# Kernel tuning notes

Measured on AMD Instinct MI355X. Metric: run time of the kernel, lower is better.

The kernel has to match this reference:

```python
import jax, jax.numpy as jnp
import numpy as np

N_NODES = 50000
N_EDGES = 800000
IN_DIM = 128
HID = 128
NUM_GRAPHS = 64


def setup_inputs() -> dict:
    key = jax.random.key(0)
    ks = jax.random.split(key, 10)
    x = jax.random.normal(ks[0], (N_NODES, IN_DIM), dtype=jnp.float32)
    edge_index = jax.random.randint(ks[1], (2, N_EDGES), 0, N_NODES, dtype=jnp.int64)
    batch = jnp.sort(jax.random.randint(ks[2], (N_NODES,), 0, NUM_GRAPHS, dtype=jnp.int64))
    s = 1.0 / np.sqrt(IN_DIM)
    W0 = jax.random.uniform(ks[3], (IN_DIM, HID), jnp.float32, -s, s)
    b0 = jnp.zeros((HID,), jnp.float32)
    s = 1.0 / np.sqrt(HID)
    W1 = jax.random.uniform(ks[4], (HID, HID), jnp.float32, -s, s)
    b1 = jnp.zeros((HID,), jnp.float32)
    W2 = jax.random.uniform(ks[5], (HID, HID), jnp.float32, -s, s)
    b2 = jnp.zeros((HID,), jnp.float32)
    return {"x": x, "edge_index": edge_index, "batch": batch,
            "W0": W0, "b0": b0, "W1": W1, "b1": b1, "W2": W2, "b2": b2}


def reference(x, edge_index, batch, W0, b0, W1, b1, W2, b2):
    N = x.shape[0]
    # GCNConv: add self loops, symmetric degree normalization
    loop = jnp.arange(N, dtype=edge_index.dtype)
    src = jnp.concatenate([edge_index[0], loop])  # [E+N]
    dst = jnp.concatenate([edge_index[1], loop])
    deg = jax.ops.segment_sum(jnp.ones_like(dst, dtype=x.dtype), dst, num_segments=N)
    dinv = jnp.where(deg > 0, jax.lax.rsqrt(deg), 0.0)
    norm = (dinv[src] * dinv[dst])[:, None]  # [E+N, 1]

    def gcn_layer(h, W, b):
        h = h @ W  # [N, hid]
        agg = jax.ops.segment_sum(h[src] * norm, dst, num_segments=N)
        return agg + b

    h = jax.nn.relu(gcn_layer(x, W0, b0))
    h = jax.nn.relu(gcn_layer(h, W1, b1))
    h = jax.nn.relu(gcn_layer(h, W2, b2))
    # dropout is identity at inference (training=False)

    # global_mean_pool by batch index
    sums = jax.ops.segment_sum(h, batch, num_segments=NUM_GRAPHS)
    counts = jax.ops.segment_sum(jnp.ones((N,), h.dtype), batch, num_segments=NUM_GRAPHS)
    return sums / jnp.maximum(counts, 1.0)[:, None]
```

## Files before the change

kernel.cpp:

```cpp
#include <hip/hip_runtime.h>
#include <hip/hip_bf16.h>

#define NNODES 50000
#define NEDGES 800000
#define HIDDIM 128
#define NGRAPH 64
#define BUCKET 64

typedef __attribute__((ext_vector_type(8))) short short8;
typedef __attribute__((ext_vector_type(4))) float floatx4;
typedef __attribute__((ext_vector_type(4))) unsigned short ushortx4;
typedef __attribute__((ext_vector_type(4))) unsigned int uintx4;

__device__ __forceinline__ float bfbits2f(unsigned short u) {
    return __uint_as_float(((unsigned int)u) << 16);
}
__device__ __forceinline__ unsigned short f2bfbits(float v) {
    __hip_bfloat16 h = __float2bfloat16(v);
    return __builtin_bit_cast(unsigned short, h);
}
__device__ __forceinline__ float bflo(unsigned int w) { return __uint_as_float(w << 16); }
__device__ __forceinline__ float bfhi(unsigned int w) { return __uint_as_float(w & 0xffff0000u); }

__global__ void k_detect(const unsigned int* __restrict__ xw,
                         const unsigned int* __restrict__ eiw,
                         int* __restrict__ flags) {
    __shared__ int sh_hit, sh_zero;
    int t = threadIdx.x;
    if (t == 0) { sh_hit = 0; sh_zero = 0; }
    __syncthreads();
    if (t < 128) {
        unsigned int w = xw[t * 97 + 5];
        int e = (int)((w >> 7) & 0xFF);
        if (e >= 110 && e <= 140) atomicAdd(&sh_hit, 1);
        if (eiw[1001 + 2 * t] == 0) atomicAdd(&sh_zero, 1);
    }
    __syncthreads();
    if (t == 0) {
        flags[0] = (sh_hit >= 64) ? 1 : 0;
        flags[1] = (sh_zero >= 120) ? 1 : 0;
    }
}

__global__ void k_init(const unsigned int* __restrict__ xw,
                       const unsigned int* __restrict__ eiw,
                       int* __restrict__ flags, int* __restrict__ cnt) {
    __shared__ int sh_hit, sh_zero;
    int t = threadIdx.x;
    int i = blockIdx.x * 256 + t;
    if (i < 50176) cnt[i] = 0;
    if (blockIdx.x != 0) return;
    if (t == 0) { sh_hit = 0; sh_zero = 0; }
    __syncthreads();
    if (t < 128) {
        unsigned int w = xw[t * 97 + 5];
        int e = (int)((w >> 7) & 0xFF);
        if (e >= 110 && e <= 140) atomicAdd(&sh_hit, 1);
        if (eiw[1001 + 2 * t] == 0) atomicAdd(&sh_zero, 1);
    }
    __syncthreads();
    if (t == 0) {
        flags[0] = (sh_hit >= 64) ? 1 : 0;
        flags[1] = (sh_zero >= 120) ? 1 : 0;
    }
}

__device__ __forceinline__ int ld_idx(const int* __restrict__ p, int j, int wide) {
    return wide ? p[2 * j] : p[j];
}

__global__ __launch_bounds__(256) void k_append(const int* __restrict__ ei,
                                                const int* __restrict__ bat,
                                                const int* __restrict__ flags,
                                                int* __restrict__ cnt,
                                                unsigned short* __restrict__ ecol,
                                                int* __restrict__ bounds) {
    if (blockIdx.x == gridDim.x - 1) {
        int g = threadIdx.x;
        if (g > NGRAPH) return;
        int wide = flags[1];
        int lo = 0, hi = NNODES;
        while (lo < hi) {
            int mid = (lo + hi) >> 1;
            if (ld_idx(bat, mid, wide) < g) lo = mid + 1; else hi = mid;
        }
        bounds[g] = lo;
        return;
    }
    int T = blockIdx.x * 256 + threadIdx.x;
    int e0 = T * 8;
    if (e0 >= NEDGES) return;
    int wide = flags[1];
    int s[8], d[8];
    if (wide) {
        const int4* __restrict__ sp = (const int4*)ei;
        const int4* __restrict__ dp = (const int4*)(ei + 2 * NEDGES);
#pragma unroll
        for (int q = 0; q < 4; ++q) {
            int4 sv = sp[T * 4 + q]; s[2 * q] = sv.x; s[2 * q + 1] = sv.z;
            int4 dv = dp[T * 4 + q]; d[2 * q] = dv.x; d[2 * q + 1] = dv.z;
        }
    } else {
        const int4* __restrict__ sp = (const int4*)ei;
        const int4* __restrict__ dp = (const int4*)(ei + NEDGES);
#pragma unroll
        for (int q = 0; q < 2; ++q) {
            int4 sv = sp[T * 2 + q];
            s[4 * q] = sv.x; s[4 * q + 1] = sv.y; s[4 * q + 2] = sv.z; s[4 * q + 3] = sv.w;
            int4 dv = dp[T * 2 + q];
            d[4 * q] = dv.x; d[4 * q + 1] = dv.y; d[4 * q + 2] = dv.z; d[4 * q + 3] = dv.w;
        }
    }
    int p[8];
#pragma unroll
    for (int q = 0; q < 8; ++q) p[q] = atomicAdd(&cnt[d[q]], 1);
#pragma unroll
    for (int q = 0; q < 8; ++q) {
        if (p[q] < BUCKET) {
            __builtin_nontemporal_store((unsigned short)s[q],
                                        &ecol[(size_t)d[q] * BUCKET + p[q]]);
        }
    }
}

__global__ __launch_bounds__(256) void k_gemm_mfma(const void* __restrict__ A,
                                                   const void* __restrict__ W,
                                                   const int* __restrict__ flags,
                                                   int a_mode,
                                                   const int* __restrict__ degcnt,
                                                   unsigned short* __restrict__ out,
                                                   int M) {
    __shared__ __align__(16) unsigned short Wl[16 * 128 * 8];
    __shared__ __align__(16) unsigned short Alds[64 * 17 * 8];
    const int tid = threadIdx.x;
    const int F = flags[0];
    const int abf = (a_mode == 2) ? 1 : (a_mode == 1 ? F : 0);
    const int row0 = blockIdx.x * 64;

    if (F) {
        const ushort4* __restrict__ Wg = (const ushort4*)W;
#pragma unroll
        for (int it = 0; it < 16; ++it) {
            int idx = it * 256 + tid;
            int k = idx >> 5, n = (idx & 31) * 4;
            ushort4 wv = Wg[idx];
            unsigned short* dst = &Wl[(((k >> 3) * 128) + n) * 8 + (k & 7)];
            dst[0] = wv.x; dst[8] = wv.y; dst[16] = wv.z; dst[24] = wv.w;
        }
    } else {
        const float4* __restrict__ Wg = (const float4*)W;
#pragma unroll
        for (int it = 0; it < 16; ++it) {
            int idx = it * 256 + tid;
            int k = idx >> 5, n = (idx & 31) * 4;
            float4 wv = Wg[idx];
            unsigned short* dst = &Wl[(((k >> 3) * 128) + n) * 8 + (k & 7)];
            dst[0] = f2bfbits(wv.x); dst[8]  = f2bfbits(wv.y);
            dst[16] = f2bfbits(wv.z); dst[24] = f2bfbits(wv.w);
        }
    }
    if (abf) {
#pragma unroll
        for (int it = 0; it < 4; ++it) {
            int idx = it * 256 + tid;
            int m = idx >> 4, kb = idx & 15;
            int gr = row0 + m;
            uint4 v = make_uint4(0, 0, 0, 0);
            if (gr < M) v = ((const uint4*)A)[(size_t)gr * 16 + kb];
            *reinterpret_cast<uint4*>(&Alds[(m * 17 + kb) * 8]) = v;
        }
    } else {
#pragma unroll
        for (int it = 0; it < 8; ++it) {
            int idx = it * 256 + tid;
            int m = idx >> 5, k4 = idx & 31;
            int k = k4 * 4;
            int gr = row0 + m;
            float4 v = make_float4(0, 0, 0, 0);
            if (gr < M) v = ((const float4*)A)[(size_t)gr * 32 + k4];
            ushort4 u;
            u.x = f2bfbits(v.x); u.y = f2bfbits(v.y);
            u.z = f2bfbits(v.z); u.w = f2bfbits(v.w);
            *reinterpret_cast<ushort4*>(&Alds[(m * 17 + (k >> 3)) * 8 + (k & 7)]) = u;
        }
    }
    __syncthreads();

    const int lane = tid & 63;
    const int wave = tid >> 6;
    const int q = lane >> 4;
    const int c = lane & 15;
    const int mrow = wave * 16 + c;
    floatx4 acc[8] = {};
#pragma unroll
    for (int k0 = 0; k0 < 4; ++k0) {
        int kb = k0 * 4 + q;
        short8 afrag = *reinterpret_cast<const short8*>(&Alds[(mrow * 17 + kb) * 8]);
#pragma unroll
        for (int t = 0; t < 8; ++t) {
            short8 bfrag = *reinterpret_cast<const short8*>(&Wl[(kb * 128 + t * 16 + c) * 8]);
            acc[t] = __builtin_amdgcn_mfma_f32_16x16x32_bf16(afrag, bfrag, acc[t], 0, 0, 0);
        }
    }
#pragma unroll
    for (int i = 0; i < 4; ++i) {
        int gr = row0 + wave * 16 + q * 4 + i;
        if (gr < M) {
            float s = degcnt ? rsqrtf((float)degcnt[gr] + 1.0f) : 1.0f;
#pragma unroll
            for (int t = 0; t < 8; ++t) {
                out[(size_t)gr * 128 + t * 16 + c] = f2bfbits(acc[t][i] * s);
            }
        }
    }
}

__global__ __launch_bounds__(256) void k_fused(const int* __restrict__ cnt,
                                               const unsigned short* __restrict__ ecol,
                                               const unsigned short* __restrict__ tmp16,
                                               const void* __restrict__ bias,
                                               const void* __restrict__ W,
                                               const int* __restrict__ flags,
                                               unsigned short* __restrict__ out,
                                               int M) {
    __shared__ __align__(16) unsigned short Wl[16 * 128 * 8];
    __shared__ __align__(16) unsigned short Alds[64 * 17 * 8];
    const int tid = threadIdx.x;
    const int F = flags[0];
    const int row0 = blockIdx.x * 64;

    if (F) {
        const ushort4* __restrict__ Wg = (const ushort4*)W;
#pragma unroll
        for (int it = 0; it < 16; ++it) {
            int idx = it * 256 + tid;
            int k = idx >> 5, n = (idx & 31) * 4;
            ushort4 wv = Wg[idx];
            unsigned short* dst = &Wl[(((k >> 3) * 128) + n) * 8 + (k & 7)];
            dst[0] = wv.x; dst[8] = wv.y; dst[16] = wv.z; dst[24] = wv.w;
        }
    } else {
        const float4* __restrict__ Wg = (const float4*)W;
#pragma unroll
        for (int it = 0; it < 16; ++it) {
            int idx = it * 256 + tid;
            int k = idx >> 5, n = (idx & 31) * 4;
            float4 wv = Wg[idx];
            unsigned short* dst = &Wl[(((k >> 3) * 128) + n) * 8 + (k & 7)];
            dst[0] = f2bfbits(wv.x); dst[8]  = f2bfbits(wv.y);
            dst[16] = f2bfbits(wv.z); dst[24] = f2bfbits(wv.w);
        }
    }

    {
        const uint4* __restrict__ base = reinterpret_cast<const uint4*>(tmp16);
        const int jl = tid & 15;
        const int nsub = tid >> 4;
        float b[8];
        if (F) {
            uint4 bb = ((const uint4*)bias)[jl];
            b[0] = bflo(bb.x); b[1] = bfhi(bb.x);
            b[2] = bflo(bb.y); b[3] = bfhi(bb.y);
            b[4] = bflo(bb.z); b[5] = bfhi(bb.z);
            b[6] = bflo(bb.w); b[7] = bfhi(bb.w);
        } else {
            float4 f0 = ((const float4*)bias)[2 * jl];
            float4 f1 = ((const float4*)bias)[2 * jl + 1];
            b[0] = f0.x; b[1] = f0.y; b[2] = f0.z; b[3] = f0.w;
            b[4] = f1.x; b[5] = f1.y; b[6] = f1.z; b[7] = f1.w;
        }
#pragma unroll
        for (int grp = 0; grp < 4; ++grp) {
            int m = grp * 16 + nsub;
            int n = row0 + m;
            float a[8] = {0, 0, 0, 0, 0, 0, 0, 0};
            float dn = 1.0f;
            bool live = (n < M);
            if (live) {
                int degf = cnt[n];
                dn = rsqrtf((float)degf + 1.0f);
                int deg = degf > BUCKET ? BUCKET : degf;
                const unsigned short* __restrict__ bk = &ecol[(size_t)n * BUCKET];
                uint4 u = base[(size_t)n * 16 + jl];
                a[0] = bflo(u.x); a[1] = bfhi(u.x);
                a[2] = bflo(u.y); a[3] = bfhi(u.y);
                a[4] = bflo(u.z); a[5] = bfhi(u.z);
                a[6] = bflo(u.w); a[7] = bfhi(u.w);
                int k = 0;
                for (; k + 3 < deg; k += 4) {
                    ushortx4 sv = __builtin_nontemporal_load(
                        reinterpret_cast<const ushortx4*>(&bk[k]));
                    uint4 u0 = base[(size_t)sv[0] * 16 + jl];
                    uint4 u1 = base[(size_t)sv[1] * 16 + jl];
                    uint4 u2 = base[(size_t)sv[2] * 16 + jl];
                    uint4 u3 = base[(size_t)sv[3] * 16 + jl];
                    a[0] += (bflo(u0.x) + bflo(u1.x)) + (bflo(u2.x) + bflo(u3.x));
                    a[1] += (bfhi(u0.x) + bfhi(u1.x)) + (bfhi(u2.x) + bfhi(u3.x));
                    a[2] += (bflo(u0.y) + bflo(u1.y)) + (bflo(u2.y) + bflo(u3.y));
                    a[3] += (bfhi(u0.y) + bfhi(u1.y)) + (bfhi(u2.y) + bfhi(u3.y));
                    a[4] += (bflo(u0.z) + bflo(u1.z)) + (bflo(u2.z) + bflo(u3.z));
                    a[5] += (bfhi(u0.z) + bfhi(u1.z)) + (bfhi(u2.z) + bfhi(u3.z));
                    a[6] += (bflo(u0.w) + bflo(u1.w)) + (bflo(u2.w) + bflo(u3.w));
                    a[7] += (bfhi(u0.w) + bfhi(u1.w)) + (bfhi(u2.w) + bfhi(u3.w));
                }
                for (; k < deg; ++k) {
                    uint4 u0 = base[(size_t)bk[k] * 16 + jl];
                    a[0] += bflo(u0.x); a[1] += bfhi(u0.x);
                    a[2] += bflo(u0.y); a[3] += bfhi(u0.y);
                    a[4] += bflo(u0.z); a[5] += bfhi(u0.z);
                    a[6] += bflo(u0.w); a[7] += bfhi(u0.w);
                }
            }
            unsigned int ow[4];
#pragma unroll
            for (int i2 = 0; i2 < 4; ++i2) {
                float r0 = live ? fmaxf(a[2 * i2]     * dn + b[2 * i2],     0.0f) : 0.0f;
                float r1 = live ? fmaxf(a[2 * i2 + 1] * dn + b[2 * i2 + 1], 0.0f) : 0.0f;
                ow[i2] = (unsigned int)f2bfbits(r0) | ((unsigned int)f2bfbits(r1) << 16);
            }
            *reinterpret_cast<uint4*>(&Alds[(m * 17 + jl) * 8]) =
                make_uint4(ow[0], ow[1], ow[2], ow[3]);
        }
    }
    __syncthreads();

    const int lane = tid & 63;
    const int wave = tid >> 6;
    const int q = lane >> 4;
    const int c = lane & 15;
    const int mrow = wave * 16 + c;
    floatx4 acc[8] = {};
#pragma unroll
    for (int k0 = 0; k0 < 4; ++k0) {
        int kb = k0 * 4 + q;
        short8 afrag = *reinterpret_cast<const short8*>(&Alds[(mrow * 17 + kb) * 8]);
#pragma unroll
        for (int t = 0; t < 8; ++t) {
            short8 bfrag = *reinterpret_cast<const short8*>(&Wl[(kb * 128 + t * 16 + c) * 8]);
            acc[t] = __builtin_amdgcn_mfma_f32_16x16x32_bf16(afrag, bfrag, acc[t], 0, 0, 0);
        }
    }
#pragma unroll
    for (int i = 0; i < 4; ++i) {
        int gr = row0 + wave * 16 + q * 4 + i;
        if (gr < M) {
            float s = rsqrtf((float)cnt[gr] + 1.0f);
#pragma unroll
            for (int t = 0; t < 8; ++t) {
                out[(size_t)gr * 128 + t * 16 + c] = f2bfbits(acc[t][i] * s);
            }
        }
    }
}

__global__ __launch_bounds__(256) void k_gather(const int* __restrict__ cnt,
                                                const unsigned short* __restrict__ ecol,
                                                const unsigned short* __restrict__ tmp16,
                                                const void* __restrict__ bias,
                                                const int* __restrict__ flags,
                                                unsigned short* __restrict__ outh16) {
    int t = blockIdx.x * 256 + threadIdx.x;
    int n = t >> 4;
    if (n >= NNODES) return;
    int j = t & 15;
    int degf = cnt[n];
    float dn = rsqrtf((float)degf + 1.0f);
    int deg = degf > BUCKET ? BUCKET : degf;
    const unsigned short* __restrict__ bk = &ecol[(size_t)n * BUCKET];
    const uint4* __restrict__ base = reinterpret_cast<const uint4*>(tmp16);
    float a[8];
    {
        uint4 u = base[(size_t)n * 16 + j];
        a[0] = bflo(u.x); a[1] = bfhi(u.x);
        a[2] = bflo(u.y); a[3] = bfhi(u.y);
        a[4] = bflo(u.z); a[5] = bfhi(u.z);
        a[6] = bflo(u.w); a[7] = bfhi(u.w);
    }
    int k = 0;
    for (; k + 3 < deg; k += 4) {
        ushortx4 sv = __builtin_nontemporal_load(
            reinterpret_cast<const ushortx4*>(&bk[k]));
        uint4 u0 = base[(size_t)sv[0] * 16 + j];
        uint4 u1 = base[(size_t)sv[1] * 16 + j];
        uint4 u2 = base[(size_t)sv[2] * 16 + j];
        uint4 u3 = base[(size_t)sv[3] * 16 + j];
        a[0] += (bflo(u0.x) + bflo(u1.x)) + (bflo(u2.x) + bflo(u3.x));
        a[1] += (bfhi(u0.x) + bfhi(u1.x)) + (bfhi(u2.x) + bfhi(u3.x));
        a[2] += (bflo(u0.y) + bflo(u1.y)) + (bflo(u2.y) + bflo(u3.y));
        a[3] += (bfhi(u0.y) + bfhi(u1.y)) + (bfhi(u2.y) + bfhi(u3.y));
        a[4] += (bflo(u0.z) + bflo(u1.z)) + (bflo(u2.z) + bflo(u3.z));
        a[5] += (bfhi(u0.z) + bfhi(u1.z)) + (bfhi(u2.z) + bfhi(u3.z));
        a[6] += (bflo(u0.w) + bflo(u1.w)) + (bflo(u2.w) + bflo(u3.w));
        a[7] += (bfhi(u0.w) + bfhi(u1.w)) + (bfhi(u2.w) + bfhi(u3.w));
    }
    for (; k < deg; ++k) {
        uint4 u0 = base[(size_t)bk[k] * 16 + j];
        a[0] += bflo(u0.x); a[1] += bfhi(u0.x);
        a[2] += bflo(u0.y); a[3] += bfhi(u0.y);
        a[4] += bflo(u0.z); a[5] += bfhi(u0.z);
        a[6] += bflo(u0.w); a[7] += bfhi(u0.w);
    }
    float b[8];
    if (flags[0]) {
        uint4 bb = ((const uint4*)bias)[j];
        b[0] = bflo(bb.x); b[1] = bfhi(bb.x);
        b[2] = bflo(bb.y); b[3] = bfhi(bb.y);
        b[4] = bflo(bb.z); b[5] = bfhi(bb.z);
        b[6] = bflo(bb.w); b[7] = bfhi(bb.w);
    } else {
        float4 f0 = ((const float4*)bias)[2 * j];
        float4 f1 = ((const float4*)bias)[2 * j + 1];
        b[0] = f0.x; b[1] = f0.y; b[2] = f0.z; b[3] = f0.w;
        b[4] = f1.x; b[5] = f1.y; b[6] = f1.z; b[7] = f1.w;
    }
    uintx4 ov;
#pragma unroll
    for (int i2 = 0; i2 < 4; ++i2) {
        float r0 = fmaxf(a[2 * i2]     * dn + b[2 * i2],     0.0f);
        float r1 = fmaxf(a[2 * i2 + 1] * dn + b[2 * i2 + 1], 0.0f);
        ov[i2] = (unsigned int)f2bfbits(r0) | ((unsigned int)f2bfbits(r1) << 16);
    }
    __builtin_nontemporal_store(ov,
        reinterpret_cast<uintx4*>(outh16 + (size_t)n * 128 + j * 8));
}

__global__ __launch_bounds__(256) void k_gemm(const void* __restrict__ A,
                                              const void* __restrict__ W,
                                              const int* __restrict__ flags,
                                              int a_uses_flag,
                                              float* __restrict__ out, int M) {
    __shared__ __align__(16) float Al[32 * 128];
    const int tid = threadIdx.x;
    const int F = flags[0];
    const int afmt = a_uses_flag ? F : 0;
    const int row0 = blockIdx.x * 32;
#pragma unroll
    for (int j = 0; j < 16; ++j) {
        int idx = j * 256 + tid;
        int r = idx >> 7, k = idx & 127;
        int gr = row0 + r;
        float v = 0.0f;
        if (gr < M) {
            size_t off = (size_t)gr * 128 + k;
            v = afmt ? bfbits2f(((const unsigned short*)A)[off])
                     : ((const float*)A)[off];
        }
        Al[idx] = v;
    }
    __syncthreads();
    const int tx = tid & 31, ty = tid >> 5;
    const int c0 = tx * 4;
    float acc[4][4] = {};
    if (F) {
        const ushort4* __restrict__ Wg = (const ushort4*)W;
#pragma unroll 4
        for (int k = 0; k < 128; ++k) {
            ushort4 wv = Wg[k * 32 + tx];
            float w0 = bfbits2f(wv.x), w1 = bfbits2f(wv.y);
            float w2 = bfbits2f(wv.z), w3 = bfbits2f(wv.w);
#pragma unroll
            for (int i = 0; i < 4; ++i) {
                float a = Al[(ty + i * 8) * 128 + k];
                acc[i][0] = fmaf(a, w0, acc[i][0]);
                acc[i][1] = fmaf(a, w1, acc[i][1]);
                acc[i][2] = fmaf(a, w2, acc[i][2]);
                acc[i][3] = fmaf(a, w3, acc[i][3]);
            }
        }
    } else {
        const float4* __restrict__ Wg = (const float4*)W;
#pragma unroll 4
        for (int k = 0; k < 128; ++k) {
            float4 wv = Wg[k * 32 + tx];
#pragma unroll
            for (int i = 0; i < 4; ++i) {
                float a = Al[(ty + i * 8) * 128 + k];
                acc[i][0] = fmaf(a, wv.x, acc[i][0]);
                acc[i][1] = fmaf(a, wv.y, acc[i][1]);
                acc[i][2] = fmaf(a, wv.z, acc[i][2]);
                acc[i][3] = fmaf(a, wv.w, acc[i][3]);
            }
        }
    }
#pragma unroll
    for (int i = 0; i < 4; ++i) {
        int gr = row0 + ty + i * 8;
        if (gr < M) {
            *reinterpret_cast<float4*>(&out[(size_t)gr * 128 + c0]) =
                make_float4(acc[i][0], acc[i][1], acc[i][2], acc[i][3]);
        }
    }
}
__global__ void k_deg_init(float* __restrict__ deg) {
    int i = blockIdx.x * 256 + threadIdx.x;
    if (i < NNODES) deg[i] = 1.0f;
}
__global__ void k_deg_edges(const int* __restrict__ ei, const int* __restrict__ flags,
                            float* __restrict__ deg) {
    int e = blockIdx.x * 256 + threadIdx.x;
    if (e < NEDGES) unsafeAtomicAdd(&deg[ld_idx(ei, NEDGES + e, flags[1])], 1.0f);
}
__global__ void k_rsqrt(float* __restrict__ deg) {
    int i = blockIdx.x * 256 + threadIdx.x;
    if (i < NNODES) deg[i] = 1.0f / sqrtf(deg[i]);
}
__global__ void k_selfloop(const float* __restrict__ tmp, const float* __restrict__ dinv,
                           float* __restrict__ agg) {
    int t = blockIdx.x * 256 + threadIdx.x;
    if (t >= NNODES * 32) return;
    int n = t >> 5, j = t & 31;
    float s = dinv[n]; s = s * s;
    float4 v = *reinterpret_cast<const float4*>(&tmp[(size_t)n * 128 + j * 4]);
    v.x *= s; v.y *= s; v.z *= s; v.w *= s;
    *reinterpret_cast<float4*>(&agg[(size_t)n * 128 + j * 4]) = v;
}
__global__ __launch_bounds__(256) void k_scatter(const int* __restrict__ ei,
                                                 const int* __restrict__ flags,
                                                 const float* __restrict__ dinv,
                                                 const float* __restrict__ tmp,
                                                 float* __restrict__ agg) {
    int t = blockIdx.x * 256 + threadIdx.x;
    int e = t >> 5;
    if (e >= NEDGES) return;
    int j = t & 31;
    int wide = flags[1];
    int s = ld_idx(ei, e, wide);
    int d = ld_idx(ei, NEDGES + e, wide);
    float w = dinv[s] * dinv[d];
    const float4 v = *reinterpret_cast<const float4*>(&tmp[(size_t)s * 128 + j * 4]);
    float* p = &agg[(size_t)d * 128 + j * 4];
    unsafeAtomicAdd(p + 0, v.x * w);
    unsafeAtomicAdd(p + 1, v.y * w);
    unsafeAtomicAdd(p + 2, v.z * w);
    unsafeAtomicAdd(p + 3, v.w * w);
}
__global__ void k_bias_relu(float* __restrict__ h, const void* __restrict__ b,
                            const int* __restrict__ flags) {
    int t = blockIdx.x * 256 + threadIdx.x;
    if (t >= NNODES * 32) return;
    int j = t & 31;
    float b0, b1, b2, b3;
    if (flags[0]) {
        const unsigned short* bb = (const unsigned short*)b;
        b0 = bfbits2f(bb[j * 4 + 0]); b1 = bfbits2f(bb[j * 4 + 1]);
        b2 = bfbits2f(bb[j * 4 + 2]); b3 = bfbits2f(bb[j * 4 + 3]);
    } else {
        const float* bb = (const float*)b;
        b0 = bb[j * 4 + 0]; b1 = bb[j * 4 + 1]; b2 = bb[j * 4 + 2]; b3 = bb[j * 4 + 3];
    }
    float4 v = *reinterpret_cast<float4*>(&h[(size_t)t * 4]);
    v.x = fmaxf(v.x + b0, 0.0f);
    v.y = fmaxf(v.y + b1, 0.0f);
    v.z = fmaxf(v.z + b2, 0.0f);
    v.w = fmaxf(v.w + b3, 0.0f);
    *reinterpret_cast<float4*>(&h[(size_t)t * 4]) = v;
}

__global__ void k_bounds(const int* __restrict__ batch, const int* __restrict__ flags,
                         int* __restrict__ bounds) {
    int g = threadIdx.x;
    if (g > NGRAPH) return;
    int wide = flags[1];
    int lo = 0, hi = NNODES;
    while (lo < hi) {
        int mid = (lo + hi) >> 1;
        if (ld_idx(batch, mid, wide) < g) lo = mid + 1; else hi = mid;
    }
    bounds[g] = lo;
}

__global__ __launch_bounds__(256) void k_pool_part(const unsigned short* __restrict__ h16,
                                                   const int* __restrict__ bounds,
                                                   float* __restrict__ part) {
    __shared__ float sh[256 * 4];
    int g = blockIdx.x >> 2, seg = blockIdx.x & 3;
    int t = threadIdx.x;
    int c4 = t & 31, sub = t >> 5;
    int beg = bounds[g], end = bounds[g + 1];
    const ushort4* __restrict__ base = (const ushort4*)h16;
    float ax = 0, ay = 0, az = 0, aw = 0;
    for (int r = beg + seg * 8 + sub; r < end; r += 32) {
        ushort4 u = base[(size_t)r * 32 + c4];
        ax += bfbits2f(u.x); ay += bfbits2f(u.y);
        az += bfbits2f(u.z); aw += bfbits2f(u.w);
    }
    sh[t * 4 + 0] = ax; sh[t * 4 + 1] = ay; sh[t * 4 + 2] = az; sh[t * 4 + 3] = aw;
    __syncthreads();
    if (t < 32) {
        float4 r = make_float4(0, 0, 0, 0);
#pragma unroll
        for (int s = 0; s < 8; ++s) {
            r.x += sh[(s * 32 + t) * 4 + 0];
            r.y += sh[(s * 32 + t) * 4 + 1];
            r.z += sh[(s * 32 + t) * 4 + 2];
            r.w += sh[(s * 32 + t) * 4 + 3];
        }
        *reinterpret_cast<float4*>(&part[((size_t)(g * 4 + seg)) * 128 + t * 4]) = r;
    }
}

__global__ void k_pool_final(const float* __restrict__ part, const int* __restrict__ bounds,
                             const int* __restrict__ flags, void* __restrict__ out) {
    int i = blockIdx.x * 256 + threadIdx.x;
    if (i >= NGRAPH * 128) return;
    int g = i >> 7, col = i & 127;
    float s = part[(g * 4 + 0) * 128 + col] + part[(g * 4 + 1) * 128 + col] +
              part[(g * 4 + 2) * 128 + col] + part[(g * 4 + 3) * 128 + col];
    float c = (float)(bounds[g + 1] - bounds[g]);
    float r = s / fmaxf(c, 1.0f);
    if (flags[0]) ((__hip_bfloat16*)out)[i] = __float2bfloat16(r);
    else          ((float*)out)[i] = r;
}

__global__ __launch_bounds__(1024) void k_pool2(const float* __restrict__ h,
                                                const int* __restrict__ bounds,
                                                const int* __restrict__ flags,
                                                void* __restrict__ out) {
    __shared__ float sh[1024];
    int g = blockIdx.x;
    int t = threadIdx.x;
    int beg = bounds[g], end = bounds[g + 1];
    int col = t & 127, seg = t >> 7;
    float acc = 0.0f;
    for (int r = beg + seg; r < end; r += 8)
        acc += h[(size_t)r * 128 + col];
    sh[t] = acc;
    __syncthreads();
    if (t < 128) {
        float total = 0.0f;
#pragma unroll
        for (int i = 0; i < 8; ++i) total += sh[t + 128 * i];
        float c = (float)(end - beg);
        float r = total / fmaxf(c, 1.0f);
        if (flags[0]) ((__hip_bfloat16*)out)[g * 128 + t] = __float2bfloat16(r);
        else          ((float*)out)[g * 128 + t] = r;
    }
}

extern "C" void kernel_launch(void* const* d_in, const int* in_sizes, int n_in,
                              void* d_out, int out_size, void* d_ws, size_t ws_size,
                              hipStream_t stream) {
    const void* x  = d_in[0];
    const int* ei  = (const int*)d_in[1];
    const int* bat = (const int*)d_in[2];
    const void* W0 = d_in[3];
    const void* b0 = d_in[4];
    const void* W1 = d_in[5];
    const void* b1 = d_in[6];
    const void* W2 = d_in[7];
    const void* b2 = d_in[8];

    float* ws = (float*)d_ws;
    size_t off = 0;
    int*   flags  = (int*)ws;           off += 16;
    float* dinv   = ws + off;           off += 50176;
    float* hA     = ws + off;           off += (size_t)NNODES * 128;
    float* hB     = ws + off;           off += (size_t)NNODES * 128;
    int*   bounds = (int*)(ws + off);   off += 80;
    int*   cnt    = (int*)(ws + off);   off += 50304;
    float* part   = ws + off;           off += NGRAPH * 4 * 128 + 64;
    const size_t needed = off * 4;
    unsigned short* hA16 = (unsigned short*)hA;
    unsigned short* hB16 = (unsigned short*)hB;
    unsigned short* ecol = (unsigned short*)(hA + (size_t)NNODES * 64);

    const int bN  = (NNODES + 255) / 256;
    const int bE  = (NEDGES + 255) / 256;
    const int bNF = (NNODES * 32) / 256;
    const int bEF = (NEDGES * 32) / 256;
    const int bA8 = (NEDGES / 8 + 255) / 256;
    const int bGT = (NNODES * 16) / 256;
    const int bG  = (NNODES + 31) / 32;
    const int bG2 = (NNODES + 63) / 64;
    dim3 blk(256);

    const bool use_csr = (ws_size >= needed);

    if (use_csr) {
        hipLaunchKernelGGL(k_init, dim3(bN), blk, 0, stream,
                           (const unsigned int*)x, (const unsigned int*)ei, flags, cnt);
        hipLaunchKernelGGL(k_append, dim3(bA8 + 1), blk, 0, stream,
                           ei, bat, flags, cnt, ecol, bounds);

        hipLaunchKernelGGL(k_gemm_mfma, dim3(bG2), blk, 0, stream, x, W0, flags, 1, cnt, hA16, NNODES);
        hipLaunchKernelGGL(k_fused, dim3(bG2), blk, 0, stream, cnt, ecol, hA16, b0, W1, flags, hB16, NNODES);
        hipLaunchKernelGGL(k_fused, dim3(bG2), blk, 0, stream, cnt, ecol, hB16, b1, W2, flags, hA16, NNODES);
        hipLaunchKernelGGL(k_gather, dim3(bGT), blk, 0, stream, cnt, ecol, hA16, b2, flags, hB16);

        hipLaunchKernelGGL(k_pool_part, dim3(NGRAPH * 4), blk, 0, stream, hB16, bounds, part);
        hipLaunchKernelGGL(k_pool_final, dim3(32), blk, 0, stream, part, bounds, flags, d_out);
    } else {
        hipLaunchKernelGGL(k_detect, dim3(1), blk, 0, stream,
                           (const unsigned int*)x, (const unsigned int*)ei, flags);
        hipLaunchKernelGGL(k_deg_init, dim3(bN), blk, 0, stream, dinv);
        hipLaunchKernelGGL(k_deg_edges, dim3(bE), blk, 0, stream, ei, flags, dinv);
        hipLaunchKernelGGL(k_rsqrt, dim3(bN), blk, 0, stream, dinv);

        hipLaunchKernelGGL(k_gemm, dim3(bG), blk, 0, stream, x, W0, flags, 1, hA, NNODES);
        hipLaunchKernelGGL(k_selfloop, dim3(bNF), blk, 0, stream, hA, dinv, hB);
        hipLaunchKernelGGL(k_scatter, dim3(bEF), blk, 0, stream, ei, flags, dinv, hA, hB);
        hipLaunchKernelGGL(k_bias_relu, dim3(bNF), blk, 0, stream, hB, b0, flags);

        hipLaunchKernelGGL(k_gemm, dim3(bG), blk, 0, stream, hB, W1, flags, 0, hA, NNODES);
        hipLaunchKernelGGL(k_selfloop, dim3(bNF), blk, 0, stream, hA, dinv, hB);
        hipLaunchKernelGGL(k_scatter, dim3(bEF), blk, 0, stream, ei, flags, dinv, hA, hB);
        hipLaunchKernelGGL(k_bias_relu, dim3(bNF), blk, 0, stream, hB, b1, flags);

        hipLaunchKernelGGL(k_gemm, dim3(bG), blk, 0, stream, hB, W2, flags, 0, hA, NNODES);
        hipLaunchKernelGGL(k_selfloop, dim3(bNF), blk, 0, stream, hA, dinv, hB);
        hipLaunchKernelGGL(k_scatter, dim3(bEF), blk, 0, stream, ei, flags, dinv, hA, hB);
        hipLaunchKernelGGL(k_bias_relu, dim3(bNF), blk, 0, stream, hB, b2, flags);

        hipLaunchKernelGGL(k_bounds, dim3(1), dim3(128), 0, stream, bat, flags, bounds);
        hipLaunchKernelGGL(k_pool2, dim3(NGRAPH), dim3(1024), 0, stream, hB, bounds, flags, d_out);
    }
}
```

Baseline: 341.4 us.

## Merge edge bucketing with first GEMM and unfuse gather from later GEMMs

The edge-append/bucketing work and the first-layer GEMM now run in one launch, with the two jobs split by block index. The layer-0 GEMM no longer scales by the degree term; instead the first gather applies per-source rsqrt weights on the fly. The fused gather+GEMM kernels are replaced by separate gather and MFMA GEMM launches, and the gather loop is unrolled to 8 neighbors with wider index loads. The intent is to overlap the atomic bucketing with GEMM work and give the gather more memory-level parallelism. The cost is extra launches and extra intermediate round trips through memory. There is also a race risk: the GEMM blocks do not read cnt, but the first gather does, and it runs only in the next launch, so that path is safe.

```diff
diff --git a/kernel.cpp b/kernel.cpp
--- a/kernel.cpp
+++ b/kernel.cpp
@@ -9,7 +9,6 @@
 
 typedef __attribute__((ext_vector_type(8))) short short8;
 typedef __attribute__((ext_vector_type(4))) float floatx4;
-typedef __attribute__((ext_vector_type(4))) unsigned short ushortx4;
 typedef __attribute__((ext_vector_type(4))) unsigned int uintx4;
 
 __device__ __forceinline__ float bfbits2f(unsigned short u) {
@@ -21,6 +20,19 @@
 }
 __device__ __forceinline__ float bflo(unsigned int w) { return __uint_as_float(w << 16); }
 __device__ __forceinline__ float bfhi(unsigned int w) { return __uint_as_float(w & 0xffff0000u); }
+
+__device__ __forceinline__ void acc8w(float* __restrict__ a, uint4 r, float wt) {
+    a[0] = fmaf(wt, bflo(r.x), a[0]); a[1] = fmaf(wt, bfhi(r.x), a[1]);
+    a[2] = fmaf(wt, bflo(r.y), a[2]); a[3] = fmaf(wt, bfhi(r.y), a[3]);
+    a[4] = fmaf(wt, bflo(r.z), a[4]); a[5] = fmaf(wt, bfhi(r.z), a[5]);
+    a[6] = fmaf(wt, bflo(r.w), a[6]); a[7] = fmaf(wt, bfhi(r.w), a[7]);
+}
+__device__ __forceinline__ void acc8p(float* __restrict__ a, uint4 r) {
+    a[0] += bflo(r.x); a[1] += bfhi(r.x);
+    a[2] += bflo(r.y); a[3] += bfhi(r.y);
+    a[4] += bflo(r.z); a[5] += bfhi(r.z);
+    a[6] += bflo(r.w); a[7] += bfhi(r.w);
+}
 
 __global__ void k_detect(const unsigned int* __restrict__ xw,
                          const unsigned int* __restrict__ eiw,
@@ -69,56 +81,145 @@
     return wide ? p[2 * j] : p[j];
 }
 
-__global__ __launch_bounds__(256) void k_append(const int* __restrict__ ei,
-                                                const int* __restrict__ bat,
-                                                const int* __restrict__ flags,
-                                                int* __restrict__ cnt,
-                                                unsigned short* __restrict__ ecol,
-                                                int* __restrict__ bounds) {
-    if (blockIdx.x == gridDim.x - 1) {
-        int g = threadIdx.x;
-        if (g > NGRAPH) return;
+__global__ __launch_bounds__(256) void k_g0a(const int* __restrict__ ei,
+                                             const int* __restrict__ bat,
+                                             const int* __restrict__ flags,
+                                             int* __restrict__ cnt,
+                                             unsigned short* __restrict__ ecol,
+                                             int* __restrict__ bounds,
+                                             const void* __restrict__ A,
+                                             const void* __restrict__ W,
+                                             unsigned short* __restrict__ out,
+                                             int M) {
+    __shared__ __align__(16) unsigned short Wl[16 * 128 * 8];
+    __shared__ __align__(16) unsigned short Alds[64 * 17 * 8];
+    const int tid = threadIdx.x;
+    const int F = flags[0];
+
+    if (blockIdx.x < 392) {
+        if (blockIdx.x == 391) {
+            int g = tid;
+            if (g > NGRAPH) return;
+            int wide = flags[1];
+            int lo = 0, hi = NNODES;
+            while (lo < hi) {
+                int mid = (lo + hi) >> 1;
+                if (ld_idx(bat, mid, wide) < g) lo = mid + 1; else hi = mid;
+            }
+            bounds[g] = lo;
+            return;
+        }
+        int T = blockIdx.x * 256 + tid;
+        int e0 = T * 8;
+        if (e0 >= NEDGES) return;
         int wide = flags[1];
-        int lo = 0, hi = NNODES;
-        while (lo < hi) {
-            int mid = (lo + hi) >> 1;
-            if (ld_idx(bat, mid, wide) < g) lo = mid + 1; else hi = mid;
-        }
-        bounds[g] = lo;
+        int s[8], d[8];
+        if (wide) {
+            const int4* __restrict__ sp = (const int4*)ei;
+            const int4* __restrict__ dp = (const int4*)(ei + 2 * NEDGES);
+#pragma unroll
+            for (int q = 0; q < 4; ++q) {
+                int4 sv = sp[T * 4 + q]; s[2 * q] = sv.x; s[2 * q + 1] = sv.z;
+                int4 dv = dp[T * 4 + q]; d[2 * q] = dv.x; d[2 * q + 1] = dv.z;
+            }
+        } else {
+            const int4* __restrict__ sp = (const int4*)ei;
+            const int4* __restrict__ dp = (const int4*)(ei + NEDGES);
+#pragma unroll
+            for (int q = 0; q < 2; ++q) {
+                int4 sv = sp[T * 2 + q];
+                s[4 * q] = sv.x; s[4 * q + 1] = sv.y; s[4 * q + 2] = sv.z; s[4 * q + 3] = sv.w;
+                int4 dv = dp[T * 2 + q];
+                d[4 * q] = dv.x; d[4 * q + 1] = dv.y; d[4 * q + 2] = dv.z; d[4 * q + 3] = dv.w;
+            }
+        }
+        int p[8];
+#pragma unroll
+        for (int q = 0; q < 8; ++q) p[q] = atomicAdd(&cnt[d[q]], 1);
+#pragma unroll
+        for (int q = 0; q < 8; ++q) {
+            if (p[q] < BUCKET) {
+                __builtin_nontemporal_store((unsigned short)s[q],
+                                            &ecol[(size_t)d[q] * BUCKET + p[q]]);
+            }
+        }
         return;
     }
-    int T = blockIdx.x * 256 + threadIdx.x;
-    int e0 = T * 8;
-    if (e0 >= NEDGES) return;
-    int wide = flags[1];
-    int s[8], d[8];
-    if (wide) {
-        const int4* __restrict__ sp = (const int4*)ei;
-        const int4* __restrict__ dp = (const int4*)(ei + 2 * NEDGES);
-#pragma unroll
-        for (int q = 0; q < 4; ++q) {
-            int4 sv = sp[T * 4 + q]; s[2 * q] = sv.x; s[2 * q + 1] = sv.z;
-            int4 dv = dp[T * 4 + q]; d[2 * q] = dv.x; d[2 * q + 1] = dv.z;
-        }
-    } else {
-        const int4* __restrict__ sp = (const int4*)ei;
-        const int4* __restrict__ dp = (const int4*)(ei + NEDGES);
-#pragma unroll
-        for (int q = 0; q < 2; ++q) {
-            int4 sv = sp[T * 2 + q];
-            s[4 * q] = sv.x; s[4 * q + 1] = sv.y; s[4 * q + 2] = sv.z; s[4 * q + 3] = sv.w;
-            int4 dv = dp[T * 2 + q];
-            d[4 * q] = dv.x; d[4 * q + 1] = dv.y; d[4 * q + 2] = dv.z; d[4 * q + 3] = dv.w;
-        }
-    }
-    int p[8];
-#pragma unroll
-    for (int q = 0; q < 8; ++q) p[q] = atomicAdd(&cnt[d[q]], 1);
-#pragma unroll
-    for (int q = 0; q < 8; ++q) {
-        if (p[q] < BUCKET) {
-            __builtin_nontemporal_store((unsigned short)s[q],
-                                        &ecol[(size_t)d[q] * BUCKET + p[q]]);
+
+    const int row0 = (blockIdx.x - 392) * 64;
+    if (F) {
+        const ushort4* __restrict__ Wg = (const ushort4*)W;
+#pragma unroll
+        for (int it = 0; it < 16; ++it) {
+            int idx = it * 256 + tid;
+            int k = idx >> 5, n = (idx & 31) * 4;
+            ushort4 wv = Wg[idx];
+            unsigned short* dst = &Wl[(((k >> 3) * 128) + n) * 8 + (k & 7)];
+            dst[0] = wv.x; dst[8] = wv.y; dst[16] = wv.z; dst[24] = wv.w;
+        }
+    } else {
+        const float4* __restrict__ Wg = (const float4*)W;
+#pragma unroll
+        for (int it = 0; it < 16; ++it) {
+            int idx = it * 256 + tid;
+            int k = idx >> 5, n = (idx & 31) * 4;
+            float4 wv = Wg[idx];
+            unsigned short* dst = &Wl[(((k >> 3) * 128) + n) * 8 + (k & 7)];
+            dst[0] = f2bfbits(wv.x); dst[8]  = f2bfbits(wv.y);
+            dst[16] = f2bfbits(wv.z); dst[24] = f2bfbits(wv.w);
+        }
+    }
+    if (F) {
+#pragma unroll
+        for (int it = 0; it < 4; ++it) {
+            int idx = it * 256 + tid;
+            int m = idx >> 4, kb = idx & 15;
+            int gr = row0 + m;
+            uint4 v = make_uint4(0, 0, 0, 0);
+            if (gr < M) v = ((const uint4*)A)[(size_t)gr * 16 + kb];
+            *reinterpret_cast<uint4*>(&Alds[(m * 17 + kb) * 8]) = v;
+        }
+    } else {
+#pragma unroll
+        for (int it = 0; it < 8; ++it) {
+            int idx = it * 256 + tid;
+            int m = idx >> 5, k4 = idx & 31;
+            int k = k4 * 4;
+            int gr = row0 + m;
+            float4 v = make_float4(0, 0, 0, 0);
+            if (gr < M) v = ((const float4*)A)[(size_t)gr * 32 + k4];
+            ushort4 u;
+            u.x = f2bfbits(v.x); u.y = f2bfbits(v.y);
+            u.z = f2bfbits(v.z); u.w = f2bfbits(v.w);
+            *reinterpret_cast<ushort4*>(&Alds[(m * 17 + (k >> 3)) * 8 + (k & 7)]) = u;
+        }
+    }
+    __syncthreads();
+
+    const int lane = tid & 63;
+    const int wave = tid >> 6;
+    const int q = lane >> 4;
+    const int c = lane & 15;
+    const int mrow = wave * 16 + c;
+    floatx4 acc[8] = {};
+#pragma unroll
+    for (int k0 = 0; k0 < 4; ++k0) {
+        int kb = k0 * 4 + q;
+        short8 afrag = *reinterpret_cast<const short8*>(&Alds[(mrow * 17 + kb) * 8]);
+#pragma unroll
+        for (int t = 0; t < 8; ++t) {
+            short8 bfrag = *reinterpret_cast<const short8*>(&Wl[(kb * 128 + t * 16 + c) * 8]);
+            acc[t] = __builtin_amdgcn_mfma_f32_16x16x32_bf16(afrag, bfrag, acc[t], 0, 0, 0);
+        }
+    }
+#pragma unroll
+    for (int i = 0; i < 4; ++i) {
+        int gr = row0 + wave * 16 + q * 4 + i;
+        if (gr < M) {
+#pragma unroll
+            for (int t = 0; t < 8; ++t) {
+                out[(size_t)gr * 128 + t * 16 + c] = f2bfbits(acc[t][i]);
+            }
         }
     }
 }
@@ -215,149 +316,12 @@
     }
 }
 
-__global__ __launch_bounds__(256) void k_fused(const int* __restrict__ cnt,
-                                               const unsigned short* __restrict__ ecol,
-                                               const unsigned short* __restrict__ tmp16,
-                                               const void* __restrict__ bias,
-                                               const void* __restrict__ W,
-                                               const int* __restrict__ flags,
-                                               unsigned short* __restrict__ out,
-                                               int M) {
-    __shared__ __align__(16) unsigned short Wl[16 * 128 * 8];
-    __shared__ __align__(16) unsigned short Alds[64 * 17 * 8];
-    const int tid = threadIdx.x;
-    const int F = flags[0];
-    const int row0 = blockIdx.x * 64;
-
-    if (F) {
-        const ushort4* __restrict__ Wg = (const ushort4*)W;
-#pragma unroll
-        for (int it = 0; it < 16; ++it) {
-            int idx = it * 256 + tid;
-            int k = idx >> 5, n = (idx & 31) * 4;
-            ushort4 wv = Wg[idx];
-            unsigned short* dst = &Wl[(((k >> 3) * 128) + n) * 8 + (k & 7)];
-            dst[0] = wv.x; dst[8] = wv.y; dst[16] = wv.z; dst[24] = wv.w;
-        }
-    } else {
-        const float4* __restrict__ Wg = (const float4*)W;
-#pragma unroll
-        for (int it = 0; it < 16; ++it) {
-            int idx = it * 256 + tid;
-            int k = idx >> 5, n = (idx & 31) * 4;
-            float4 wv = Wg[idx];
-            unsigned short* dst = &Wl[(((k >> 3) * 128) + n) * 8 + (k & 7)];
-            dst[0] = f2bfbits(wv.x); dst[8]  = f2bfbits(wv.y);
-            dst[16] = f2bfbits(wv.z); dst[24] = f2bfbits(wv.w);
-        }
-    }
-
-    {
-        const uint4* __restrict__ base = reinterpret_cast<const uint4*>(tmp16);
-        const int jl = tid & 15;
-        const int nsub = tid >> 4;
-        float b[8];
-        if (F) {
-            uint4 bb = ((const uint4*)bias)[jl];
-            b[0] = bflo(bb.x); b[1] = bfhi(bb.x);
-            b[2] = bflo(bb.y); b[3] = bfhi(bb.y);
-            b[4] = bflo(bb.z); b[5] = bfhi(bb.z);
-            b[6] = bflo(bb.w); b[7] = bfhi(bb.w);
-        } else {
-            float4 f0 = ((const float4*)bias)[2 * jl];
-            float4 f1 = ((const float4*)bias)[2 * jl + 1];
-            b[0] = f0.x; b[1] = f0.y; b[2] = f0.z; b[3] = f0.w;
-            b[4] = f1.x; b[5] = f1.y; b[6] = f1.z; b[7] = f1.w;
-        }
-#pragma unroll
-        for (int grp = 0; grp < 4; ++grp) {
-            int m = grp * 16 + nsub;
-            int n = row0 + m;
-            float a[8] = {0, 0, 0, 0, 0, 0, 0, 0};
-            float dn = 1.0f;
-            bool live = (n < M);
-            if (live) {
-                int degf = cnt[n];
-                dn = rsqrtf((float)degf + 1.0f);
-                int deg = degf > BUCKET ? BUCKET : degf;
-                const unsigned short* __restrict__ bk = &ecol[(size_t)n * BUCKET];
-                uint4 u = base[(size_t)n * 16 + jl];
-                a[0] = bflo(u.x); a[1] = bfhi(u.x);
-                a[2] = bflo(u.y); a[3] = bfhi(u.y);
-                a[4] = bflo(u.z); a[5] = bfhi(u.z);
-                a[6] = bflo(u.w); a[7] = bfhi(u.w);
-                int k = 0;
-                for (; k + 3 < deg; k += 4) {
-                    ushortx4 sv = __builtin_nontemporal_load(
-                        reinterpret_cast<const ushortx4*>(&bk[k]));
-                    uint4 u0 = base[(size_t)sv[0] * 16 + jl];
-                    uint4 u1 = base[(size_t)sv[1] * 16 + jl];
-                    uint4 u2 = base[(size_t)sv[2] * 16 + jl];
-                    uint4 u3 = base[(size_t)sv[3] * 16 + jl];
-                    a[0] += (bflo(u0.x) + bflo(u1.x)) + (bflo(u2.x) + bflo(u3.x));
-                    a[1] += (bfhi(u0.x) + bfhi(u1.x)) + (bfhi(u2.x) + bfhi(u3.x));
-                    a[2] += (bflo(u0.y) + bflo(u1.y)) + (bflo(u2.y) + bflo(u3.y));
-                    a[3] += (bfhi(u0.y) + bfhi(u1.y)) + (bfhi(u2.y) + bfhi(u3.y));
-                    a[4] += (bflo(u0.z) + bflo(u1.z)) + (bflo(u2.z) + bflo(u3.z));
-                    a[5] += (bfhi(u0.z) + bfhi(u1.z)) + (bfhi(u2.z) + bfhi(u3.z));
-                    a[6] += (bflo(u0.w) + bflo(u1.w)) + (bflo(u2.w) + bflo(u3.w));
-                    a[7] += (bfhi(u0.w) + bfhi(u1.w)) + (bfhi(u2.w) + bfhi(u3.w));
-                }
-                for (; k < deg; ++k) {
-                    uint4 u0 = base[(size_t)bk[k] * 16 + jl];
-                    a[0] += bflo(u0.x); a[1] += bfhi(u0.x);
-                    a[2] += bflo(u0.y); a[3] += bfhi(u0.y);
-                    a[4] += bflo(u0.z); a[5] += bfhi(u0.z);
-                    a[6] += bflo(u0.w); a[7] += bfhi(u0.w);
-                }
-            }
-            unsigned int ow[4];
-#pragma unroll
-            for (int i2 = 0; i2 < 4; ++i2) {
-                float r0 = live ? fmaxf(a[2 * i2]     * dn + b[2 * i2],     0.0f) : 0.0f;
-                float r1 = live ? fmaxf(a[2 * i2 + 1] * dn + b[2 * i2 + 1], 0.0f) : 0.0f;
-                ow[i2] = (unsigned int)f2bfbits(r0) | ((unsigned int)f2bfbits(r1) << 16);
-            }
-            *reinterpret_cast<uint4*>(&Alds[(m * 17 + jl) * 8]) =
-                make_uint4(ow[0], ow[1], ow[2], ow[3]);
-        }
-    }
-    __syncthreads();
-
-    const int lane = tid & 63;
-    const int wave = tid >> 6;
-    const int q = lane >> 4;
-    const int c = lane & 15;
-    const int mrow = wave * 16 + c;
-    floatx4 acc[8] = {};
-#pragma unroll
-    for (int k0 = 0; k0 < 4; ++k0) {
-        int kb = k0 * 4 + q;
-        short8 afrag = *reinterpret_cast<const short8*>(&Alds[(mrow * 17 + kb) * 8]);
-#pragma unroll
-        for (int t = 0; t < 8; ++t) {
-            short8 bfrag = *reinterpret_cast<const short8*>(&Wl[(kb * 128 + t * 16 + c) * 8]);
-            acc[t] = __builtin_amdgcn_mfma_f32_16x16x32_bf16(afrag, bfrag, acc[t], 0, 0, 0);
-        }
-    }
-#pragma unroll
-    for (int i = 0; i < 4; ++i) {
-        int gr = row0 + wave * 16 + q * 4 + i;
-        if (gr < M) {
-            float s = rsqrtf((float)cnt[gr] + 1.0f);
-#pragma unroll
-            for (int t = 0; t < 8; ++t) {
-                out[(size_t)gr * 128 + t * 16 + c] = f2bfbits(acc[t][i] * s);
-            }
-        }
-    }
-}
-
 __global__ __launch_bounds__(256) void k_gather(const int* __restrict__ cnt,
                                                 const unsigned short* __restrict__ ecol,
                                                 const unsigned short* __restrict__ tmp16,
                                                 const void* __restrict__ bias,
                                                 const int* __restrict__ flags,
+                                                const int* __restrict__ scl,
                                                 unsigned short* __restrict__ outh16) {
     int t = blockIdx.x * 256 + threadIdx.x;
     int n = t >> 4;
@@ -371,34 +335,87 @@
     float a[8];
     {
         uint4 u = base[(size_t)n * 16 + j];
-        a[0] = bflo(u.x); a[1] = bfhi(u.x);
-        a[2] = bflo(u.y); a[3] = bfhi(u.y);
-        a[4] = bflo(u.z); a[5] = bfhi(u.z);
-        a[6] = bflo(u.w); a[7] = bfhi(u.w);
+        float w0 = scl ? dn : 1.0f;
+        a[0] = w0 * bflo(u.x); a[1] = w0 * bfhi(u.x);
+        a[2] = w0 * bflo(u.y); a[3] = w0 * bfhi(u.y);
+        a[4] = w0 * bflo(u.z); a[5] = w0 * bfhi(u.z);
+        a[6] = w0 * bflo(u.w); a[7] = w0 * bfhi(u.w);
     }
     int k = 0;
-    for (; k + 3 < deg; k += 4) {
-        ushortx4 sv = __builtin_nontemporal_load(
-            reinterpret_cast<const ushortx4*>(&bk[k]));
-        uint4 u0 = base[(size_t)sv[0] * 16 + j];
-        uint4 u1 = base[(size_t)sv[1] * 16 + j];
-        uint4 u2 = base[(size_t)sv[2] * 16 + j];
-        uint4 u3 = base[(size_t)sv[3] * 16 + j];
-        a[0] += (bflo(u0.x) + bflo(u1.x)) + (bflo(u2.x) + bflo(u3.x));
-        a[1] += (bfhi(u0.x) + bfhi(u1.x)) + (bfhi(u2.x) + bfhi(u3.x));
-        a[2] += (bflo(u0.y) + bflo(u1.y)) + (bflo(u2.y) + bflo(u3.y));
-        a[3] += (bfhi(u0.y) + bfhi(u1.y)) + (bfhi(u2.y) + bfhi(u3.y));
-        a[4] += (bflo(u0.z) + bflo(u1.z)) + (bflo(u2.z) + bflo(u3.z));
-        a[5] += (bfhi(u0.z) + bfhi(u1.z)) + (bfhi(u2.z) + bfhi(u3.z));
-        a[6] += (bflo(u0.w) + bflo(u1.w)) + (bflo(u2.w) + bflo(u3.w));
-        a[7] += (bfhi(u0.w) + bfhi(u1.w)) + (bfhi(u2.w) + bfhi(u3.w));
-    }
-    for (; k < deg; ++k) {
-        uint4 u0 = base[(size_t)bk[k] * 16 + j];
-        a[0] += bflo(u0.x); a[1] += bfhi(u0.x);
-        a[2] += bflo(u0.y); a[3] += bfhi(u0.y);
-        a[4] += bflo(u0.z); a[5] += bfhi(u0.z);
-        a[6] += bflo(u0.w); a[7] += bfhi(u0.w);
+    if (scl) {
+        for (; k + 7 < deg; k += 8) {
+            uint4 bw = *reinterpret_cast<const uint4*>(&bk[k]);
+            int s0 = bw.x & 0xffff, s1 = bw.x >> 16;
+            int s2 = bw.y & 0xffff, s3 = bw.y >> 16;
+            int s4 = bw.z & 0xffff, s5 = bw.z >> 16;
+            int s6 = bw.w & 0xffff, s7 = bw.w >> 16;
+            uint4 r0 = base[(size_t)s0 * 16 + j];
+            uint4 r1 = base[(size_t)s1 * 16 + j];
+            uint4 r2 = base[(size_t)s2 * 16 + j];
+            uint4 r3 = base[(size_t)s3 * 16 + j];
+            uint4 r4 = base[(size_t)s4 * 16 + j];
+            uint4 r5 = base[(size_t)s5 * 16 + j];
+            uint4 r6 = base[(size_t)s6 * 16 + j];
+            uint4 r7 = base[(size_t)s7 * 16 + j];
+            acc8w(a, r0, rsqrtf((float)scl[s0] + 1.0f));
+            acc8w(a, r1, rsqrtf((float)scl[s1] + 1.0f));
+            acc8w(a, r2, rsqrtf((float)scl[s2] + 1.0f));
+            acc8w(a, r3, rsqrtf((float)scl[s3] + 1.0f));
+            acc8w(a, r4, rsqrtf((float)scl[s4] + 1.0f));
+            acc8w(a, r5, rsqrtf((float)scl[s5] + 1.0f));
+            acc8w(a, r6, rsqrtf((float)scl[s6] + 1.0f));
+            acc8w(a, r7, rsqrtf((float)scl[s7] + 1.0f));
+        }
+        for (; k + 3 < deg; k += 4) {
+            uint2 bw = *reinterpret_cast<const uint2*>(&bk[k]);
+            int s0 = bw.x & 0xffff, s1 = bw.x >> 16;
+            int s2 = bw.y & 0xffff, s3 = bw.y >> 16;
+            uint4 r0 = base[(size_t)s0 * 16 + j];
+            uint4 r1 = base[(size_t)s1 * 16 + j];
+            uint4 r2 = base[(size_t)s2 * 16 + j];
+            uint4 r3 = base[(size_t)s3 * 16 + j];
+            acc8w(a, r0, rsqrtf((float)scl[s0] + 1.0f));
+            acc8w(a, r1, rsqrtf((float)scl[s1] + 1.0f));
+            acc8w(a, r2, rsqrtf((float)scl[s2] + 1.0f));
+            acc8w(a, r3, rsqrtf((float)scl[s3] + 1.0f));
+        }
+        for (; k < deg; ++k) {
+            int s0 = bk[k];
+            uint4 r0 = base[(size_t)s0 * 16 + j];
+            acc8w(a, r0, rsqrtf((float)scl[s0] + 1.0f));
+        }
+    } else {
+        for (; k + 7 < deg; k += 8) {
+            uint4 bw = *reinterpret_cast<const uint4*>(&bk[k]);
+            int s0 = bw.x & 0xffff, s1 = bw.x >> 16;
+            int s2 = bw.y & 0xffff, s3 = bw.y >> 16;
+            int s4 = bw.z & 0xffff, s5 = bw.z >> 16;
+            int s6 = bw.w & 0xffff, s7 = bw.w >> 16;
+            uint4 r0 = base[(size_t)s0 * 16 + j];
+            uint4 r1 = base[(size_t)s1 * 16 + j];
+            uint4 r2 = base[(size_t)s2 * 16 + j];
+            uint4 r3 = base[(size_t)s3 * 16 + j];
+            uint4 r4 = base[(size_t)s4 * 16 + j];
+            uint4 r5 = base[(size_t)s5 * 16 + j];
+            uint4 r6 = base[(size_t)s6 * 16 + j];
+            uint4 r7 = base[(size_t)s7 * 16 + j];
+            acc8p(a, r0); acc8p(a, r1); acc8p(a, r2); acc8p(a, r3);
+            acc8p(a, r4); acc8p(a, r5); acc8p(a, r6); acc8p(a, r7);
+        }
+        for (; k + 3 < deg; k += 4) {
+            uint2 bw = *reinterpret_cast<const uint2*>(&bk[k]);
+            int s0 = bw.x & 0xffff, s1 = bw.x >> 16;
+            int s2 = bw.y & 0xffff, s3 = bw.y >> 16;
+            uint4 r0 = base[(size_t)s0 * 16 + j];
+            uint4 r1 = base[(size_t)s1 * 16 + j];
+            uint4 r2 = base[(size_t)s2 * 16 + j];
+            uint4 r3 = base[(size_t)s3 * 16 + j];
+            acc8p(a, r0); acc8p(a, r1); acc8p(a, r2); acc8p(a, r3);
+        }
+        for (; k < deg; ++k) {
+            uint4 r0 = base[(size_t)bk[k] * 16 + j];
+            acc8p(a, r0);
+        }
     }
     float b[8];
     if (flags[0]) {
@@ -668,7 +685,6 @@
     const int bE  = (NEDGES + 255) / 256;
     const int bNF = (NNODES * 32) / 256;
     const int bEF = (NEDGES * 32) / 256;
-    const int bA8 = (NEDGES / 8 + 255) / 256;
     const int bGT = (NNODES * 16) / 256;
     const int bG  = (NNODES + 31) / 32;
     const int bG2 = (NNODES + 63) / 64;
@@ -679,13 +695,14 @@
     if (use_csr) {
         hipLaunchKernelGGL(k_init, dim3(bN), blk, 0, stream,
                            (const unsigned int*)x, (const unsigned int*)ei, flags, cnt);
-        hipLaunchKernelGGL(k_append, dim3(bA8 + 1), blk, 0, stream,
-                           ei, bat, flags, cnt, ecol, bounds);
-
-        hipLaunchKernelGGL(k_gemm_mfma, dim3(bG2), blk, 0, stream, x, W0, flags, 1, cnt, hA16, NNODES);
-        hipLaunchKernelGGL(k_fused, dim3(bG2), blk, 0, stream, cnt, ecol, hA16, b0, W1, flags, hB16, NNODES);
-        hipLaunchKernelGGL(k_fused, dim3(bG2), blk, 0, stream, cnt, ecol, hB16, b1, W2, flags, hA16, NNODES);
-        hipLaunchKernelGGL(k_gather, dim3(bGT), blk, 0, stream, cnt, ecol, hA16, b2, flags, hB16);
+        hipLaunchKernelGGL(k_g0a, dim3(392 + bG2), blk, 0, stream,
+                           ei, bat, flags, cnt, ecol, bounds, x, W0, hA16, NNODES);
+
+        hipLaunchKernelGGL(k_gather, dim3(bGT), blk, 0, stream, cnt, ecol, hA16, b0, flags, cnt, hB16);
+        hipLaunchKernelGGL(k_gemm_mfma, dim3(bG2), blk, 0, stream, hB16, W1, flags, 2, cnt, hA16, NNODES);
+        hipLaunchKernelGGL(k_gather, dim3(bGT), blk, 0, stream, cnt, ecol, hA16, b1, flags, (const int*)nullptr, hB16);
+        hipLaunchKernelGGL(k_gemm_mfma, dim3(bG2), blk, 0, stream, hB16, W2, flags, 2, cnt, hA16, NNODES);
+        hipLaunchKernelGGL(k_gather, dim3(bGT), blk, 0, stream, cnt, ecol, hA16, b2, flags, (const int*)nullptr, hB16);
 
         hipLaunchKernelGGL(k_pool_part, dim3(NGRAPH * 4), blk, 0, stream, hB16, bounds, part);
         hipLaunchKernelGGL(k_pool_final, dim3(32), blk, 0, stream, part, bounds, flags, d_out);
```

After: 320.2 us. 1.07x faster.
